# Performance work log

Hardware: AMD Instinct MI355X
Metric: run time of the kernel (lower is better)

The kernel has to match this reference:

```python
import jax, jax.numpy as jnp
import numpy as np

B = 16384

def setup_inputs() -> dict:
    key = jax.random.key(0)
    k1, k2, k3 = jax.random.split(key, 3)
    predictions = jax.random.uniform(k1, (B, 7 * 7 * 30), dtype=jnp.float32)
    targets = jax.random.uniform(k2, (B, 7 * 7 * 25), dtype=jnp.float32)
    # channel 4 of each grid cell is the object-present indicator, compared to exactly 1
    t = targets.reshape(B, 7, 7, 25)
    present = (jax.random.uniform(k3, (B, 7, 7)) > 0.5).astype(jnp.float32)
    t = t.at[..., 4].set(present)
    targets = t.reshape(B, 7 * 7 * 25)
    return {"predictions": predictions, "targets": targets}


def reference(predictions, targets):
    num_batches = predictions.shape[0]
    p = predictions.reshape(num_batches, 7, 7, 30)
    t = targets.reshape(num_batches, 7, 7, 25)

    c1 = p[..., 4]
    c2 = p[..., 9]
    c = t[..., 4]
    present = (c == 1.0)
    responsible1 = c1 > c2  # box 1 is responsible

    # objectiveness loss
    obj_present = jnp.where(responsible1, jnp.square(c1 - c), jnp.square(c2 - c))
    obj_absent = 0.5 * (jnp.square(c1) + jnp.square(c2))
    obj_loss = jnp.sum(jnp.where(present, obj_present, obj_absent))

    # classification loss (only where object present)
    cls_sq = jnp.sum(jnp.square(p[..., 10:30] - t[..., 5:25]), axis=-1)  # [B,7,7]
    class_loss = jnp.sum(jnp.where(present, cls_sq, 0.0))

    r = responsible1[..., None]
    p_center = jnp.where(r, p[..., 0:2], p[..., 5:7])
    p_hw = jnp.where(r, p[..., 2:4], p[..., 7:9])
    t_center = t[..., 0:2]
    t_hw = t[..., 2:4]
    box_sq = (jnp.sum(jnp.square(p_center - t_center), axis=-1)
              + jnp.sum(jnp.square(jnp.sqrt(p_hw) - jnp.sqrt(t_hw)), axis=-1))  # [B,7,7]
    box_loss = 5.0 * jnp.sum(jnp.where(present, box_sq, 0.0))

    return obj_loss + class_loss + box_loss
```

## Files before the change

kernel.cpp:

```cpp
#include <hip/hip_runtime.h>
#include <stdint.h>


#define TPB    128
#define CELLS  128
#define NTILES 6272
#define GRID   1568
#define KTILES 4
#define P_F4   960
#define T_F4   800

#define GL2LDS(gptr, lptr)                                                    \
    __builtin_amdgcn_global_load_lds(                                         \
        (const __attribute__((address_space(1))) void*)(gptr),                \
        (__attribute__((address_space(3))) void*)(uintptr_t)(lptr), 16, 0, 0)

__global__ __launch_bounds__(TPB) void yolo_loss_kernel(
    const float* __restrict__ pred,
    const float* __restrict__ targ,
    float* __restrict__ out)
{
    __shared__ float4 sp4[P_F4];
    __shared__ float4 st4[T_F4];

    const int tid = threadIdx.x;
    const float* sp = (const float*)sp4;
    const float* st = (const float*)st4;

    float loss = 0.0f;
    int tile = blockIdx.x;

    for (int j = 0; j < KTILES; ++j) {
        const float4* gp = (const float4*)pred + (size_t)tile * P_F4;
        const float4* gt = (const float4*)targ + (size_t)tile * T_F4;
        #pragma unroll
        for (int r = 0; r < 7; ++r) GL2LDS(gp + tid + r * TPB, sp4 + tid + r * TPB);
        if (tid < 64)               GL2LDS(gp + 896 + tid,     sp4 + 896 + tid);
        #pragma unroll
        for (int r = 0; r < 6; ++r) GL2LDS(gt + tid + r * TPB, st4 + tid + r * TPB);
        if (tid < 32)               GL2LDS(gt + 768 + tid,     st4 + 768 + tid);

        __syncthreads();

        const float2* pv2 = (const float2*)(sp + tid * 30);
        float pv[30];
        #pragma unroll
        for (int i = 0; i < 15; ++i) {
            float2 v = pv2[i];
            pv[2*i] = v.x; pv[2*i+1] = v.y;
        }
        const float* tvp = st + tid * 25;
        float tv[25];
        #pragma unroll
        for (int i = 0; i < 25; ++i) tv[i] = tvp[i];

        float c1 = pv[4], c2 = pv[9], cc = tv[4];
        bool present = (cc == 1.0f);
        bool resp1   = (c1 > c2);

        float d1 = c1 - cc, d2 = c2 - cc;
        float obj_present = resp1 ? d1 * d1 : d2 * d2;
        float obj_absent  = 0.5f * (c1 * c1 + c2 * c2);
        float obj = present ? obj_present : obj_absent;

        float cls = 0.0f;
        #pragma unroll
        for (int k = 0; k < 20; ++k) {
            float d = pv[10 + k] - tv[5 + k];
            cls += d * d;
        }

        float pc0 = resp1 ? pv[0] : pv[5];
        float pc1 = resp1 ? pv[1] : pv[6];
        float ph0 = resp1 ? pv[2] : pv[7];
        float ph1 = resp1 ? pv[3] : pv[8];
        float b0 = pc0 - tv[0];
        float b1 = pc1 - tv[1];
        float s0 = sqrtf(ph0) - sqrtf(tv[2]);
        float s1 = sqrtf(ph1) - sqrtf(tv[3]);
        float box = b0 * b0 + b1 * b1 + s0 * s0 + s1 * s1;

        loss += obj + (present ? (cls + 5.0f * box) : 0.0f);

        __syncthreads();
        tile += GRID;
    }

    #pragma unroll
    for (int off = 32; off > 0; off >>= 1)
        loss += __shfl_down(loss, off);

    __shared__ float warp_sums[TPB / 64];
    if ((tid & 63) == 0) warp_sums[tid >> 6] = loss;
    __syncthreads();

    if (tid == 0)
        atomicAdd(out, warp_sums[0] + warp_sums[1]);
}

extern "C" void kernel_launch(void* const* d_in, const int* in_sizes, int n_in,
                              void* d_out, int out_size, void* d_ws, size_t ws_size,
                              hipStream_t stream)
{
    const float* pred = (const float*)d_in[0];
    const float* targ = (const float*)d_in[1];
    float* out = (float*)d_out;

    hipMemsetAsync(out, 0, sizeof(float), stream);

    hipLaunchKernelGGL(yolo_loss_kernel, dim3(GRID), dim3(TPB), 0, stream,
                       pred, targ, out);
}
```

Baseline: 197.9 us.

## Double-buffer LDS tiles per single-wave block with vmcnt-based prefetch

Shrinks blocks to one 64-thread wave and gives each block 7 contiguous 64-cell tiles. Two LDS buffers are used so the async global-to-LDS loads for the next tile overlap computation on the current one, synchronised with s_waitcnt vmcnt rather than __syncthreads. The cross-warp shared reduction is dropped because each block is a single wave. The result depends on the vmcnt(15) count matching the number of issued loads per stage and on wave-level visibility of LDS writes. There is a potential hazard in reusing a buffer without a barrier.

```diff
diff --git a/kernel.cpp b/kernel.cpp
--- a/kernel.cpp
+++ b/kernel.cpp
@@ -2,13 +2,11 @@
 #include <stdint.h>
 
 
-#define TPB    128
-#define CELLS  128
-#define NTILES 6272
-#define GRID   1568
-#define KTILES 4
-#define P_F4   960
-#define T_F4   800
+#define TPB    64
+#define KT     7
+#define GRID   1792
+#define P_F4   480
+#define T_F4   400
 
 #define GL2LDS(gptr, lptr)                                                    \
     __builtin_amdgcn_global_load_lds(                                         \
@@ -20,28 +18,23 @@
     const float* __restrict__ targ,
     float* __restrict__ out)
 {
-    __shared__ float4 sp4[P_F4];
-    __shared__ float4 st4[T_F4];
+    __shared__ float4 spA[P_F4], stA[T_F4];
+    __shared__ float4 spB[P_F4], stB[T_F4];
 
     const int tid = threadIdx.x;
-    const float* sp = (const float*)sp4;
-    const float* st = (const float*)st4;
 
-    float loss = 0.0f;
-    int tile = blockIdx.x;
+    auto STAGE = [&](int t, float4* sp4, float4* st4) {
+        const float4* gp = (const float4*)pred + (size_t)t * P_F4;
+        const float4* gt = (const float4*)targ + (size_t)t * T_F4;
+        #pragma unroll
+        for (int r = 0; r < 7; ++r) GL2LDS(gp + tid + r * 64, sp4 + tid + r * 64);
+        if (tid < 32)               GL2LDS(gp + 448 + tid,    sp4 + 448 + tid);
+        #pragma unroll
+        for (int r = 0; r < 6; ++r) GL2LDS(gt + tid + r * 64, st4 + tid + r * 64);
+        if (tid < 16)               GL2LDS(gt + 384 + tid,    st4 + 384 + tid);
+    };
 
-    for (int j = 0; j < KTILES; ++j) {
-        const float4* gp = (const float4*)pred + (size_t)tile * P_F4;
-        const float4* gt = (const float4*)targ + (size_t)tile * T_F4;
-        #pragma unroll
-        for (int r = 0; r < 7; ++r) GL2LDS(gp + tid + r * TPB, sp4 + tid + r * TPB);
-        if (tid < 64)               GL2LDS(gp + 896 + tid,     sp4 + 896 + tid);
-        #pragma unroll
-        for (int r = 0; r < 6; ++r) GL2LDS(gt + tid + r * TPB, st4 + tid + r * TPB);
-        if (tid < 32)               GL2LDS(gt + 768 + tid,     st4 + 768 + tid);
-
-        __syncthreads();
-
+    auto CELL = [&](const float* sp, const float* st) -> float {
         const float2* pv2 = (const float2*)(sp + tid * 30);
         float pv[30];
         #pragma unroll
@@ -59,9 +52,8 @@
         bool resp1   = (c1 > c2);
 
         float d1 = c1 - cc, d2 = c2 - cc;
-        float obj_present = resp1 ? d1 * d1 : d2 * d2;
-        float obj_absent  = 0.5f * (c1 * c1 + c2 * c2);
-        float obj = present ? obj_present : obj_absent;
+        float obj = present ? (resp1 ? d1 * d1 : d2 * d2)
+                            : 0.5f * (c1 * c1 + c2 * c2);
 
         float cls = 0.0f;
         #pragma unroll
@@ -80,22 +72,35 @@
         float s1 = sqrtf(ph1) - sqrtf(tv[3]);
         float box = b0 * b0 + b1 * b1 + s0 * s0 + s1 * s1;
 
-        loss += obj + (present ? (cls + 5.0f * box) : 0.0f);
+        return obj + (present ? (cls + 5.0f * box) : 0.0f);
+    };
 
-        __syncthreads();
-        tile += GRID;
+    const int base = blockIdx.x * KT;
+    float loss = 0.0f;
+
+    STAGE(base, spA, stA);
+
+    #pragma unroll
+    for (int j = 0; j < KT; ++j) {
+        const bool odd = (j & 1);
+        if (j + 1 < KT) {
+            if (odd) STAGE(base + j + 1, spA, stA);
+            else     STAGE(base + j + 1, spB, stB);
+            asm volatile("s_waitcnt vmcnt(15)" ::: "memory");
+        } else {
+            asm volatile("s_waitcnt vmcnt(0)" ::: "memory");
+        }
+        __builtin_amdgcn_sched_barrier(0);
+
+        loss += odd ? CELL((const float*)spB, (const float*)stB)
+                    : CELL((const float*)spA, (const float*)stA);
     }
 
     #pragma unroll
     for (int off = 32; off > 0; off >>= 1)
         loss += __shfl_down(loss, off);
-
-    __shared__ float warp_sums[TPB / 64];
-    if ((tid & 63) == 0) warp_sums[tid >> 6] = loss;
-    __syncthreads();
-
     if (tid == 0)
-        atomicAdd(out, warp_sums[0] + warp_sums[1]);
+        atomicAdd(out, loss);
 }
 
 extern "C" void kernel_launch(void* const* d_in, const int* in_sizes, int n_in,
```

Result: slower. 204.3 us (+3.2%).
